# Performance work log

Hardware: AMD Instinct MI355X
Metric: run time of the kernel (lower is better)

Reference implementation:

```python
import jax, jax.numpy as jnp
from jax import lax
import numpy as np

NHEAD = 8
GROUPS = 32


def _conv2d(x, w, b=None, stride=1, pad=1):
    y = lax.conv_general_dilated(x, w, (stride, stride), ((pad, pad), (pad, pad)),
                                 dimension_numbers=('NCHW', 'OIHW', 'NCHW'))
    return y if b is None else y + b[None, :, None, None]


def _xcorr(x, k):
    # depthwise cross-correlation: batch*channel groups
    b, c, H, W = x.shape
    y = lax.conv_general_dilated(x.reshape(1, b * c, H, W),
                                 k.reshape(b * c, 1, k.shape[2], k.shape[3]),
                                 (1, 1), 'VALID', feature_group_count=b * c,
                                 dimension_numbers=('NCHW', 'OIHW', 'NCHW'))
    return y.reshape(b, c, y.shape[2], y.shape[3])


def _bn(x, g, b, m, v):
    inv = lax.rsqrt(v + 1e-5)
    return (x - m[None, :, None, None]) * (g * inv)[None, :, None, None] + b[None, :, None, None]


def _gn(x, g, b):
    B, C, H, W = x.shape
    xr = x.reshape(B, GROUPS, -1)
    mu = xr.mean(-1, keepdims=True)
    var = xr.var(-1, keepdims=True)
    xr = (xr - mu) * lax.rsqrt(var + 1e-5)
    return xr.reshape(B, C, H, W) * g[None, :, None, None] + b[None, :, None, None]


def _ln(x, g, b):
    mu = x.mean(-1, keepdims=True)
    var = x.var(-1, keepdims=True)
    return (x - mu) * lax.rsqrt(var + 1e-5) * g + b


def _mha(q, k, v, wq, bq, wk, bk, wv, bv, wo, bo, bias):
    N, B, C = q.shape
    D = C // NHEAD
    qh = (q @ wq.T + bq).reshape(N, B, NHEAD, D)
    kh = (k @ wk.T + bk).reshape(k.shape[0], B, NHEAD, D)
    vh = (v @ wv.T + bv).reshape(v.shape[0], B, NHEAD, D)
    att = jnp.einsum('nbhd,mbhd->bhnm', qh, kh) * (D ** -0.5)
    att = jax.nn.softmax(att + bias[None, None], axis=-1)  # local-window additive mask
    o = jnp.einsum('bhnm,mbhd->nbhd', att, vh).reshape(N, B, C)
    return o @ wo.T + bo


def _forward(mask_size, x0, x1, x2, z0, z1, z2,
             conv1_w, bn1_g, bn1_b, bn1_m, bn1_v,
             conv3_w, bn3_g, bn3_b, bn3_m, bn3_v,
             conv2_w, bn2_g, bn2_b, bn2_m, bn2_v,
             row_embed, col_embed,
             t_wq, t_bq, t_wk, t_bk, t_wv, t_bv, t_wo, t_bo,
             t_ln1_g, t_ln1_b, t_ff1_w, t_ff1_b, t_ff2_w, t_ff2_b, t_ln2_g, t_ln2_b,
             convloc_w, convloc_b, convloc_gn_g, convloc_gn_b, loc_out_w, loc_out_b,
             convcls_w, convcls_b, convcls_gn_g, convcls_gn_b,
             cls1_w, cls1_b, cls2_w, cls2_b):
    res1 = jax.nn.relu(_bn(_conv2d(_xcorr(x0, z0), conv1_w, None, 2, 1), bn1_g, bn1_b, bn1_m, bn1_v))
    res2 = jax.nn.relu(_bn(_conv2d(_xcorr(x1, z1), conv3_w, None, 2, 1), bn3_g, bn3_b, bn3_m, bn3_v))
    res3 = jax.nn.relu(_bn(_conv2d(_xcorr(x2, z2), conv2_w, None, 2, 1), bn2_g, bn2_b, bn2_m, bn2_v))

    b, c, W3, H3 = res3.shape
    # positional embedding: h,w = res3.shape[-2:]
    hh, ww = W3, H3
    x_emb = col_embed[:ww]            # (w, C/2)
    y_emb = row_embed[:hh]            # (h, C/2)
    half = c // 2
    pos_hw = jnp.concatenate([jnp.broadcast_to(x_emb[None], (hh, ww, half)),
                              jnp.broadcast_to(y_emb[:, None], (hh, ww, half))], -1)
    pos_seq = pos_hw.reshape(hh * ww, 1, c)  # (N,1,C), broadcasts over batch

    # local-window mask: position allowed iff both coord offsets <= mask_size//2
    ms2 = mask_size // 2
    idx = jnp.arange(W3 * H3)
    ri, ci = idx // H3, idx % H3
    allowed = (jnp.abs(ri[:, None] - ri[None, :]) <= ms2) & (jnp.abs(ci[:, None] - ci[None, :]) <= ms2)
    bias = jnp.where(allowed, 0.0, -1e9).astype(res3.dtype)

    src1 = res1.reshape(b, c, -1).transpose(2, 0, 1)  # (N,B,C)
    src2 = res2.reshape(b, c, -1).transpose(2, 0, 1)
    src3 = res3.reshape(b, c, -1).transpose(2, 0, 1)

    out = src3
    mems = (src1, src2)
    for li in range(2):  # 2 post-norm transformer layers (fixed structural loop)
        q = out + pos_seq
        kk = mems[li] + pos_seq
        a = _mha(q, kk, mems[li], t_wq[li], t_bq[li], t_wk[li], t_bk[li],
                 t_wv[li], t_bv[li], t_wo[li], t_bo[li], bias)
        out = _ln(out + a, t_ln1_g[li], t_ln1_b[li])
        ff = jax.nn.relu(out @ t_ff1_w[li].T + t_ff1_b[li]) @ t_ff2_w[li].T + t_ff2_b[li]
        out = _ln(out + ff, t_ln2_g[li], t_ln2_b[li])

    res = out.transpose(1, 2, 0).reshape(b, c, W3, H3)

    y = res
    for i in range(3):
        y = jax.nn.relu(_gn(_conv2d(y, convloc_w[i], convloc_b[i]), convloc_gn_g[i], convloc_gn_b[i]))
    loc = _conv2d(y, loc_out_w, loc_out_b)

    y = res
    for i in range(3):
        y = jax.nn.relu(_gn(_conv2d(y, convcls_w[i], convcls_b[i]), convcls_gn_g[i], convcls_gn_b[i]))
    cls1 = _conv2d(y, cls1_w, cls1_b)
    cls2 = _conv2d(y, cls2_w, cls2_b)
    return (loc, cls1, cls2)


def setup_inputs():
    key = jax.random.key(0)
    kit = iter(jax.random.split(key, 80))
    def nrm(shape, s=1.0):
        return (jax.random.normal(next(kit), shape) * s).astype(jnp.float32)
    def uni(shape):
        return jax.random.uniform(next(kit), shape, dtype=jnp.float32)
    d = {}
    d['x0'] = nrm((64, 384, 31, 31)); d['x1'] = nrm((64, 384, 31, 31)); d['x2'] = nrm((64, 256, 31, 31))
    d['z0'] = nrm((64, 384, 7, 7)); d['z1'] = nrm((64, 384, 7, 7)); d['z2'] = nrm((64, 256, 7, 7))
    d['conv1_w'] = nrm((192, 384, 3, 3), 0.01)
    d['conv3_w'] = nrm((192, 384, 3, 3), 0.02)
    d['conv2_w'] = nrm((192, 256, 3, 3), 0.02)
    for tag in ('1', '2', '3'):
        d['bn%s_g' % tag] = jnp.ones(192); d['bn%s_b' % tag] = jnp.zeros(192)
        d['bn%s_m' % tag] = jnp.zeros(192); d['bn%s_v' % tag] = jnp.ones(192)
    d['row_embed'] = uni((50, 96)); d['col_embed'] = uni((50, 96))
    for nm in ('q', 'k', 'v', 'o'):
        d['t_w%s' % nm] = nrm((2, 192, 192), 0.02); d['t_b%s' % nm] = jnp.zeros((2, 192))
    d['t_ln1_g'] = jnp.ones((2, 192)); d['t_ln1_b'] = jnp.zeros((2, 192))
    d['t_ln2_g'] = jnp.ones((2, 192)); d['t_ln2_b'] = jnp.zeros((2, 192))
    d['t_ff1_w'] = nrm((2, 768, 192), 0.02); d['t_ff1_b'] = jnp.zeros((2, 768))
    d['t_ff2_w'] = nrm((2, 192, 768), 0.02); d['t_ff2_b'] = jnp.zeros((2, 192))
    d['convloc_w'] = nrm((3, 192, 192, 3, 3), 0.02); d['convloc_b'] = jnp.zeros((3, 192))
    d['convloc_gn_g'] = jnp.ones((3, 192)); d['convloc_gn_b'] = jnp.zeros((3, 192))
    d['loc_out_w'] = nrm((4, 192, 3, 3), 0.02); d['loc_out_b'] = jnp.zeros(4)
    d['convcls_w'] = nrm((3, 192, 192, 3, 3), 0.02); d['convcls_b'] = jnp.zeros((3, 192))
    d['convcls_gn_g'] = jnp.ones((3, 192)); d['convcls_gn_b'] = jnp.zeros((3, 192))
    d['cls1_w'] = nrm((2, 192, 3, 3), 0.02); d['cls1_b'] = jnp.zeros(2)
    d['cls2_w'] = nrm((1, 192, 3, 3), 0.02); d['cls2_b'] = jnp.zeros(1)
    d['mask_size'] = 5
    return d


def reference(x0, x1, x2, z0, z1, z2,
              conv1_w, bn1_g, bn1_b, bn1_m, bn1_v,
              conv3_w, bn3_g, bn3_b, bn3_m, bn3_v,
              conv2_w, bn2_g, bn2_b, bn2_m, bn2_v,
              row_embed, col_embed,
              t_wq, t_bq, t_wk, t_bk, t_wv, t_bv, t_wo, t_bo,
              t_ln1_g, t_ln1_b, t_ff1_w, t_ff1_b, t_ff2_w, t_ff2_b, t_ln2_g, t_ln2_b,
              convloc_w, convloc_b, convloc_gn_g, convloc_gn_b, loc_out_w, loc_out_b,
              convcls_w, convcls_b, convcls_gn_g, convcls_gn_b,
              cls1_w, cls1_b, cls2_w, cls2_b, mask_size):
    return _forward(mask_size, x0, x1, x2, z0, z1, z2,
                    conv1_w, bn1_g, bn1_b, bn1_m, bn1_v,
                    conv3_w, bn3_g, bn3_b, bn3_m, bn3_v,
                    conv2_w, bn2_g, bn2_b, bn2_m, bn2_v,
                    row_embed, col_embed,
                    t_wq, t_bq, t_wk, t_bk, t_wv, t_bv, t_wo, t_bo,
                    t_ln1_g, t_ln1_b, t_ff1_w, t_ff1_b, t_ff2_w, t_ff2_b, t_ln2_g, t_ln2_b,
                    convloc_w, convloc_b, convloc_gn_g, convloc_gn_b, loc_out_w, loc_out_b,
                    convcls_w, convcls_b, convcls_gn_g, convcls_gn_b,
                    cls1_w, cls1_b, cls2_w, cls2_b)
```

## Files before the change

kernel.cpp:

```cpp
#include <hip/hip_runtime.h>
#include <cstdint>
#include <cstddef>

#define NB   64
#define C192 192
#define NPIX 169
#define WD   13
#define NH   8
#define HD   24
#define SEQM (NPIX*NB)

__global__ __launch_bounds__(256) void xcorr_kernel(
    const float* __restrict__ x, const float* __restrict__ z,
    float* __restrict__ out)
{
    int bc = blockIdx.x;
    const float* xin = x + (size_t)bc * 961;
    const float* zin = z + (size_t)bc * 49;
    float* o = out + (size_t)bc * 625;
    __shared__ float xs[961];
    __shared__ float zs[49];
    for (int i = threadIdx.x; i < 961; i += 256) xs[i] = xin[i];
    if (threadIdx.x < 49) zs[threadIdx.x] = zin[threadIdx.x];
    __syncthreads();
    for (int p = threadIdx.x; p < 625; p += 256) {
        int oy = p / 25, ox = p % 25;
        float acc = 0.f;
        #pragma unroll
        for (int ky = 0; ky < 7; ++ky) {
            #pragma unroll
            for (int kx = 0; kx < 7; ++kx)
                acc = fmaf(xs[(oy + ky) * 31 + ox + kx], zs[ky * 7 + kx], acc);
        }
        o[p] = acc;
    }
}

template<int CIN, int S, int HIN, bool TRANS_OUT>
__global__ __launch_bounds__(256) void conv_gemm(
    const float* __restrict__ in, const float* __restrict__ w,
    float* __restrict__ part)
{
    constexpr int KH = CIN / 2;
    constexpr int NT = KH / 4;
    __shared__ float smem[2 * 36 * 68];
    float* As = smem;
    float* Ws = smem + 36 * 68;
    const int m0 = blockIdx.x * 64;
    const int n0 = blockIdx.y * 64;
    const int kz = blockIdx.z;
    const int t  = threadIdx.x;
    const int lm = t & 63;
    const int lc = t >> 6;
    const int m  = m0 + lm;
    const int b  = m / NPIX;
    const int pix = m % NPIX;
    const int oy = pix / WD, ox = pix % WD;
    const int iy0 = S * oy - 1, ix0 = S * ox - 1;
    bool okY[3], okX[3];
    #pragma unroll
    for (int k = 0; k < 3; ++k) {
        okY[k] = (unsigned)(iy0 + k) < (unsigned)HIN;
        okX[k] = (unsigned)(ix0 + k) < (unsigned)HIN;
    }
    const float* pA = in + ((size_t)b * CIN + kz * KH + lc) * (HIN * HIN) + iy0 * HIN + ix0;
    const float* pW = w + ((size_t)(n0 + lm) * CIN + kz * KH + lc) * 9;
    const int tx = t & 15, ty = t >> 4;
    float acc[4][4] = {};
    float av[9], wv[9];
    #pragma unroll
    for (int ky = 0; ky < 3; ++ky)
        #pragma unroll
        for (int kx = 0; kx < 3; ++kx)
            av[ky * 3 + kx] = (okY[ky] && okX[kx]) ? pA[ky * HIN + kx] : 0.f;
    #pragma unroll
    for (int j = 0; j < 9; ++j) wv[j] = pW[j];

    for (int kt = 0; kt < NT; ++kt) {
        __syncthreads();
        {
            float* a  = As + (lc * 9) * 68 + lm;
            float* wd = Ws + (lc * 9) * 68 + lm;
            #pragma unroll
            for (int j = 0; j < 9; ++j) { a[j * 68] = av[j]; wd[j * 68] = wv[j]; }
        }
        __syncthreads();
        if (kt + 1 < NT) {
            pA += 4 * HIN * HIN;
            pW += 36;
            #pragma unroll
            for (int ky = 0; ky < 3; ++ky)
                #pragma unroll
                for (int kx = 0; kx < 3; ++kx)
                    av[ky * 3 + kx] = (okY[ky] && okX[kx]) ? pA[ky * HIN + kx] : 0.f;
            #pragma unroll
            for (int j = 0; j < 9; ++j) wv[j] = pW[j];
        }
        #pragma unroll
        for (int kk = 0; kk < 36; ++kk) {
            const float4 a4 = *(const float4*)&As[kk * 68 + ty * 4];
            const float4 w4 = *(const float4*)&Ws[kk * 68 + tx * 4];
            const float aa[4] = {a4.x, a4.y, a4.z, a4.w};
            const float wb[4] = {w4.x, w4.y, w4.z, w4.w};
            #pragma unroll
            for (int i = 0; i < 4; ++i)
                #pragma unroll
                for (int j = 0; j < 4; ++j)
                    acc[i][j] = fmaf(aa[i], wb[j], acc[i][j]);
        }
    }
    part += (size_t)kz * ((size_t)SEQM * C192);
    if (!TRANS_OUT) {
        #pragma unroll
        for (int i = 0; i < 4; ++i) {
            int mm = m0 + ty * 4 + i;
            float4 v = make_float4(acc[i][0], acc[i][1], acc[i][2], acc[i][3]);
            *(float4*)&part[(size_t)mm * C192 + n0 + tx * 4] = v;
        }
    } else {
        __syncthreads();
        float* Cl = smem;
        #pragma unroll
        for (int i = 0; i < 4; ++i)
            #pragma unroll
            for (int j = 0; j < 4; ++j)
                Cl[(tx * 4 + j) * 65 + ty * 4 + i] = acc[i][j];
        __syncthreads();
        #pragma unroll
        for (int rep = 0; rep < 16; ++rep) {
            int nl = rep * 4 + lc;
            part[((size_t)b * C192 + n0 + nl) * NPIX + pix] = Cl[nl * 65 + lm];
        }
    }
}

__global__ __launch_bounds__(256) void reduce_bn_relu(
    const float* __restrict__ p, const float* __restrict__ g,
    const float* __restrict__ bb, const float* __restrict__ mm,
    const float* __restrict__ vv, float* __restrict__ out)
{
    const int i = blockIdx.x * 256 + threadIdx.x;
    const int c4 = i % 48;
    const float4* p4 = (const float4*)p;
    float4 a = p4[i];
    float4 bpart = p4[i + (size_t)SEQM * 48];
    float4 g4 = *(const float4*)&g[c4 * 4];
    float4 b4 = *(const float4*)&bb[c4 * 4];
    float4 m4 = *(const float4*)&mm[c4 * 4];
    float4 v4 = *(const float4*)&vv[c4 * 4];
    float4 r;
    {
        float sc = g4.x * rsqrtf(v4.x + 1e-5f); r.x = fmaxf(fmaf(a.x + bpart.x - m4.x, sc, b4.x), 0.f);
    }
    { float sc = g4.y * rsqrtf(v4.y + 1e-5f); r.y = fmaxf(fmaf(a.y + bpart.y - m4.y, sc, b4.y), 0.f); }
    { float sc = g4.z * rsqrtf(v4.z + 1e-5f); r.z = fmaxf(fmaf(a.z + bpart.z - m4.z, sc, b4.z), 0.f); }
    { float sc = g4.w * rsqrtf(v4.w + 1e-5f); r.w = fmaxf(fmaf(a.w + bpart.w - m4.w, sc, b4.w), 0.f); }
    ((float4*)out)[i] = r;
}

__global__ __launch_bounds__(256) void gn_reduce_relu(
    const float* __restrict__ p, const float* __restrict__ cbias,
    const float* __restrict__ g, const float* __restrict__ bgn,
    float* __restrict__ out)
{
    const int blk = blockIdx.x;
    const int bb = blk / 32, grp = blk % 32;
    const size_t base = ((size_t)bb * C192 + grp * 6) * NPIX;
    const float* p0 = p + base;
    const float* p1 = p + (size_t)SEQM * C192 + base;
    const int N = 6 * NPIX;
    const int t = threadIdx.x;
    float vals[4];
    float s = 0.f, s2 = 0.f;
    #pragma unroll
    for (int i = 0; i < 4; ++i) {
        int idx = t + i * 256;
        float v = 0.f;
        if (idx < N) v = p0[idx] + p1[idx] + cbias[grp * 6 + idx / NPIX];
        vals[i] = v; s += v; s2 += v * v;
    }
    #pragma unroll
    for (int o = 32; o; o >>= 1) { s += __shfl_down(s, o); s2 += __shfl_down(s2, o); }
    __shared__ float redS[4], redS2[4];
    int wid = t >> 6, lane = t & 63;
    if (lane == 0) { redS[wid] = s; redS2[wid] = s2; }
    __syncthreads();
    float S  = redS[0] + redS[1] + redS[2] + redS[3];
    float S2 = redS2[0] + redS2[1] + redS2[2] + redS2[3];
    float mean = S / (float)N;
    float var  = S2 / (float)N - mean * mean;
    float inv  = rsqrtf(var + 1e-5f);
    #pragma unroll
    for (int i = 0; i < 4; ++i) {
        int idx = t + i * 256;
        if (idx < N) {
            int ch = grp * 6 + idx / NPIX;
            float y = (vals[i] - mean) * inv * g[ch] + bgn[ch];
            out[base + idx] = fmaxf(y, 0.f);
        }
    }
}

template<int CO_T>
__global__ __launch_bounds__(192) void conv_s1_bias(
    const float* __restrict__ in, const float* __restrict__ w,
    const float* __restrict__ bias, float* __restrict__ out)
{
    const int b    = blockIdx.x;
    const int co0  = blockIdx.y * CO_T;
    const int Cout = gridDim.y * CO_T;
    const int t    = threadIdx.x;
    __shared__ float xs[4 * 225];
    float acc[CO_T];
    #pragma unroll
    for (int i = 0; i < CO_T; ++i) acc[i] = 0.f;
    int py = 0, px = 0;
    if (t < NPIX) { py = t / WD; px = t % WD; }
    const float* inb = in + (size_t)b * C192 * NPIX;

    for (int c0 = 0; c0 < C192; c0 += 4) {
        __syncthreads();
        for (int i = t; i < 4 * 225; i += 192) {
            int pl = i / 225, pp = i % 225;
            int y = pp / 15, x = pp % 15;
            float v = 0.f;
            if (y >= 1 && y <= 13 && x >= 1 && x <= 13)
                v = inb[(size_t)(c0 + pl) * NPIX + (y - 1) * WD + (x - 1)];
            xs[i] = v;
        }
        __syncthreads();
        if (t < NPIX) {
            #pragma unroll
            for (int pl = 0; pl < 4; ++pl) {
                float xv[9];
                const float* xp = xs + pl * 225;
                #pragma unroll
                for (int ky = 0; ky < 3; ++ky) {
                    #pragma unroll
                    for (int kx = 0; kx < 3; ++kx)
                        xv[ky * 3 + kx] = xp[(py + ky) * 15 + px + kx];
                }
                #pragma unroll
                for (int co = 0; co < CO_T; ++co) {
                    const float* wc = w + ((size_t)(co0 + co) * C192 + (c0 + pl)) * 9;
                    #pragma unroll
                    for (int k = 0; k < 9; ++k)
                        acc[co] = fmaf(xv[k], wc[k], acc[co]);
                }
            }
        }
    }
    if (t < NPIX) {
        #pragma unroll
        for (int co = 0; co < CO_T; ++co) {
            int c = co0 + co;
            out[((size_t)b * Cout + c) * NPIX + t] = acc[co] + bias[c];
        }
    }
}

template<bool RELU>
__global__ __launch_bounds__(256) void gemm_nt(
    const float* __restrict__ A, const float* __restrict__ W,
    const float* __restrict__ bias, float* __restrict__ C,
    int M, int N, int K)
{
    const int BK = 32;
    __shared__ float As[BK][68];
    __shared__ float Ws[BK][68];
    const int mb = blockIdx.x, nb = blockIdx.y;
    const int t = threadIdx.x;
    const int tx = t % 16, ty = t / 16;
    float acc[4][4] = {};
    for (int k0 = 0; k0 < K; k0 += BK) {
        __syncthreads();
        {
            int r = t / 8, kv = (t % 8) * 4;
            const float4 a0 = *(const float4*)&A[(size_t)(mb * 64 + r) * K + k0 + kv];
            const float4 a1 = *(const float4*)&A[(size_t)(mb * 64 + r + 32) * K + k0 + kv];
            As[kv + 0][r] = a0.x; As[kv + 1][r] = a0.y; As[kv + 2][r] = a0.z; As[kv + 3][r] = a0.w;
            As[kv + 0][r + 32] = a1.x; As[kv + 1][r + 32] = a1.y; As[kv + 2][r + 32] = a1.z; As[kv + 3][r + 32] = a1.w;
            const float4 w0 = *(const float4*)&W[(size_t)(nb * 64 + r) * K + k0 + kv];
            const float4 w1 = *(const float4*)&W[(size_t)(nb * 64 + r + 32) * K + k0 + kv];
            Ws[kv + 0][r] = w0.x; Ws[kv + 1][r] = w0.y; Ws[kv + 2][r] = w0.z; Ws[kv + 3][r] = w0.w;
            Ws[kv + 0][r + 32] = w1.x; Ws[kv + 1][r + 32] = w1.y; Ws[kv + 2][r + 32] = w1.z; Ws[kv + 3][r + 32] = w1.w;
        }
        __syncthreads();
        #pragma unroll
        for (int kk = 0; kk < BK; ++kk) {
            const float4 a4 = *(const float4*)&As[kk][ty * 4];
            const float4 w4 = *(const float4*)&Ws[kk][tx * 4];
            const float aa[4] = {a4.x, a4.y, a4.z, a4.w};
            const float wb[4] = {w4.x, w4.y, w4.z, w4.w};
            #pragma unroll
            for (int i = 0; i < 4; ++i)
                #pragma unroll
                for (int j = 0; j < 4; ++j)
                    acc[i][j] = fmaf(aa[i], wb[j], acc[i][j]);
        }
    }
    const float4 bv = *(const float4*)&bias[nb * 64 + tx * 4];
    #pragma unroll
    for (int i = 0; i < 4; ++i) {
        int mrow = mb * 64 + ty * 4 + i;
        float4 v = make_float4(acc[i][0] + bv.x, acc[i][1] + bv.y,
                               acc[i][2] + bv.z, acc[i][3] + bv.w);
        if (RELU) { v.x = fmaxf(v.x, 0.f); v.y = fmaxf(v.y, 0.f); v.z = fmaxf(v.z, 0.f); v.w = fmaxf(v.w, 0.f); }
        *(float4*)&C[(size_t)mrow * N + nb * 64 + tx * 4] = v;
    }
}

__global__ __launch_bounds__(256) void addpos_kernel(
    const float* __restrict__ src, const float* __restrict__ row_e,
    const float* __restrict__ col_e, float* __restrict__ dst)
{
    const int total = SEQM * C192;
    int i = blockIdx.x * 256 + threadIdx.x;
    if (i >= total) return;
    int c = i % C192;
    int pix = (i / C192) % NPIX;
    float p = (c < 96) ? col_e[(pix % WD) * 96 + c] : row_e[(pix / WD) * 96 + (c - 96)];
    dst[i] = src[i] + p;
}

__global__ __launch_bounds__(192) void attn_kernel(
    const float* __restrict__ Q, const float* __restrict__ K,
    const float* __restrict__ V, const int* __restrict__ mask_size,
    float* __restrict__ O)
{
    const int bh = blockIdx.x;
    const int b = bh / NH, h = bh % NH;
    __shared__ float Ks[NPIX][HD];
    __shared__ float Vs[NPIX][HD];
    const int t = threadIdx.x;
    for (int i = t; i < NPIX * HD; i += 192) {
        int n = i / HD, d = i % HD;
        size_t base = ((size_t)b * NPIX + n) * C192 + h * HD + d;
        Ks[n][d] = K[base];
        Vs[n][d] = V[base];
    }
    __syncthreads();
    if (t < NPIX) {
        float q[HD];
        size_t qbase = ((size_t)b * NPIX + t) * C192 + h * HD;
        #pragma unroll
        for (int d = 0; d < HD; ++d) q[d] = Q[qbase + d];
        const int ms2 = mask_size[0] / 2;
        const int ri = t / WD, ci = t % WD;
        const int r0 = max(ri - ms2, 0), r1 = min(ri + ms2, WD - 1);
        const int c0 = max(ci - ms2, 0), c1 = min(ci + ms2, WD - 1);
        float mx = -1e30f, sum = 0.f;
        float o[HD];
        #pragma unroll
        for (int d = 0; d < HD; ++d) o[d] = 0.f;
        const float scale = 0.20412414523193150f;
        for (int rm = r0; rm <= r1; ++rm) {
            for (int cm = c0; cm <= c1; ++cm) {
                int m = rm * WD + cm;
                float s = 0.f;
                #pragma unroll
                for (int d = 0; d < HD; ++d) s = fmaf(q[d], Ks[m][d], s);
                s *= scale;
                if (s > mx) {
                    float f = expf(mx - s);
                    sum *= f;
                    #pragma unroll
                    for (int d = 0; d < HD; ++d) o[d] *= f;
                    mx = s;
                }
                float p = expf(s - mx);
                sum += p;
                #pragma unroll
                for (int d = 0; d < HD; ++d) o[d] = fmaf(p, Vs[m][d], o[d]);
            }
        }
        float r = 1.f / sum;
        #pragma unroll
        for (int d = 0; d < HD; ++d) O[qbase + d] = o[d] * r;
    }
}

__global__ __launch_bounds__(256) void add_ln_kernel(
    float* __restrict__ x, const float* __restrict__ a,
    const float* __restrict__ g, const float* __restrict__ b)
{
    const int row = blockIdx.x * 4 + (threadIdx.x >> 6);
    const int lane = threadIdx.x & 63;
    float* xp = x + (size_t)row * C192;
    const float* ap = a + (size_t)row * C192;
    float v[3];
    float s = 0.f, s2 = 0.f;
    #pragma unroll
    for (int i = 0; i < 3; ++i) {
        float t = xp[lane + i * 64] + ap[lane + i * 64];
        v[i] = t; s += t; s2 += t * t;
    }
    #pragma unroll
    for (int o = 32; o; o >>= 1) { s += __shfl_down(s, o); s2 += __shfl_down(s2, o); }
    s = __shfl(s, 0); s2 = __shfl(s2, 0);
    float mean = s * (1.f / 192.f);
    float var  = s2 * (1.f / 192.f) - mean * mean;
    float inv  = rsqrtf(var + 1e-5f);
    #pragma unroll
    for (int i = 0; i < 3; ++i) {
        int c = lane + i * 64;
        xp[c] = (v[i] - mean) * inv * g[c] + b[c];
    }
}

__global__ __launch_bounds__(256) void bpc_to_bcp(
    const float* __restrict__ src, float* __restrict__ dst)
{
    __shared__ float tile[32][33];
    const int b = blockIdx.z;
    const int n0 = blockIdx.x * 32, c0 = blockIdx.y * 32;
    const int tx = threadIdx.x % 32, ty = threadIdx.x / 32;
    #pragma unroll
    for (int i = 0; i < 32; i += 8) {
        int n = n0 + ty + i, c = c0 + tx;
        if (n < NPIX) tile[ty + i][tx] = src[((size_t)b * NPIX + n) * C192 + c];
    }
    __syncthreads();
    #pragma unroll
    for (int i = 0; i < 32; i += 8) {
        int c = c0 + ty + i, n = n0 + tx;
        if (n < NPIX) dst[((size_t)b * C192 + c) * NPIX + n] = tile[tx][ty + i];
    }
}

extern "C" void kernel_launch(void* const* d_in, const int* in_sizes, int n_in,
                              void* d_out, int out_size, void* d_ws, size_t ws_size,
                              hipStream_t stream)
{
    const float* x0 = (const float*)d_in[0];
    const float* x1 = (const float*)d_in[1];
    const float* x2 = (const float*)d_in[2];
    const float* z0 = (const float*)d_in[3];
    const float* z1 = (const float*)d_in[4];
    const float* z2 = (const float*)d_in[5];
    const float* conv1_w = (const float*)d_in[6];
    const float* conv3_w = (const float*)d_in[7];
    const float* conv2_w = (const float*)d_in[8];
    const float* bn1_g = (const float*)d_in[9];
    const float* bn1_b = (const float*)d_in[10];
    const float* bn1_m = (const float*)d_in[11];
    const float* bn1_v = (const float*)d_in[12];
    const float* bn2_g = (const float*)d_in[13];
    const float* bn2_b = (const float*)d_in[14];
    const float* bn2_m = (const float*)d_in[15];
    const float* bn2_v = (const float*)d_in[16];
    const float* bn3_g = (const float*)d_in[17];
    const float* bn3_b = (const float*)d_in[18];
    const float* bn3_m = (const float*)d_in[19];
    const float* bn3_v = (const float*)d_in[20];
    const float* row_embed = (const float*)d_in[21];
    const float* col_embed = (const float*)d_in[22];
    const float* t_wq = (const float*)d_in[23];
    const float* t_bq = (const float*)d_in[24];
    const float* t_wk = (const float*)d_in[25];
    const float* t_bk = (const float*)d_in[26];
    const float* t_wv = (const float*)d_in[27];
    const float* t_bv = (const float*)d_in[28];
    const float* t_wo = (const float*)d_in[29];
    const float* t_bo = (const float*)d_in[30];
    const float* t_ln1_g = (const float*)d_in[31];
    const float* t_ln1_b = (const float*)d_in[32];
    const float* t_ln2_g = (const float*)d_in[33];
    const float* t_ln2_b = (const float*)d_in[34];
    const float* t_ff1_w = (const float*)d_in[35];
    const float* t_ff1_b = (const float*)d_in[36];
    const float* t_ff2_w = (const float*)d_in[37];
    const float* t_ff2_b = (const float*)d_in[38];
    const float* convloc_w = (const float*)d_in[39];
    const float* convloc_b = (const float*)d_in[40];
    const float* convloc_gn_g = (const float*)d_in[41];
    const float* convloc_gn_b = (const float*)d_in[42];
    const float* loc_out_w = (const float*)d_in[43];
    const float* loc_out_b = (const float*)d_in[44];
    const float* convcls_w = (const float*)d_in[45];
    const float* convcls_b = (const float*)d_in[46];
    const float* convcls_gn_g = (const float*)d_in[47];
    const float* convcls_gn_b = (const float*)d_in[48];
    const float* cls1_w = (const float*)d_in[49];
    const float* cls1_b = (const float*)d_in[50];
    const float* cls2_w = (const float*)d_in[51];
    const float* cls2_b = (const float*)d_in[52];
    const int*   mask_size = (const int*)d_in[53];
    float* out = (float*)d_out;

    const size_t SZ_X = (size_t)NB * 384 * 625;
    const size_t SZ_S = (size_t)SEQM * C192;
    float* ws   = (float*)d_ws;
    float* Abuf = ws;
    float* res1 = Abuf + SZ_X;
    float* res2 = res1 + SZ_S;
    float* outb = res2 + SZ_S;
    float* qb   = outb + SZ_S;
    float* kb   = qb + SZ_S;
    float* vb   = kb + SZ_S;
    float* ob   = vb + SZ_S;
    float* resT = ob + SZ_S;
    float* y0   = resT + SZ_S;
    float* y1   = y0 + SZ_S;
    float* pbuf = qb;

    const dim3 cgrid(NPIX, 3, 2);
    const int  rgrid = SEQM * 48 / 256;
    const dim3 tgrid(6, 6, NB);

    xcorr_kernel<<<NB * 384, 256, 0, stream>>>(x0, z0, Abuf);
    conv_gemm<384, 2, 25, false><<<cgrid, 256, 0, stream>>>(Abuf, conv1_w, pbuf);
    reduce_bn_relu<<<rgrid, 256, 0, stream>>>(pbuf, bn1_g, bn1_b, bn1_m, bn1_v, res1);

    xcorr_kernel<<<NB * 384, 256, 0, stream>>>(x1, z1, Abuf);
    conv_gemm<384, 2, 25, false><<<cgrid, 256, 0, stream>>>(Abuf, conv3_w, pbuf);
    reduce_bn_relu<<<rgrid, 256, 0, stream>>>(pbuf, bn3_g, bn3_b, bn3_m, bn3_v, res2);

    xcorr_kernel<<<NB * 256, 256, 0, stream>>>(x2, z2, Abuf);
    conv_gemm<256, 2, 25, false><<<cgrid, 256, 0, stream>>>(Abuf, conv2_w, pbuf);
    reduce_bn_relu<<<rgrid, 256, 0, stream>>>(pbuf, bn2_g, bn2_b, bn2_m, bn2_v, outb);

    const int addpos_grid = (SEQM * C192 + 255) / 256;
    for (int li = 0; li < 2; ++li) {
        const float* mem = (li == 0) ? res1 : res2;
        const float* wq = t_wq + (size_t)li * C192 * C192;
        const float* wk = t_wk + (size_t)li * C192 * C192;
        const float* wv = t_wv + (size_t)li * C192 * C192;
        const float* wo = t_wo + (size_t)li * C192 * C192;
        const float* bq = t_bq + (size_t)li * C192;
        const float* bk = t_bk + (size_t)li * C192;
        const float* bv = t_bv + (size_t)li * C192;
        const float* bo = t_bo + (size_t)li * C192;

        addpos_kernel<<<addpos_grid, 256, 0, stream>>>(outb, row_embed, col_embed, qb);
        addpos_kernel<<<addpos_grid, 256, 0, stream>>>(mem,  row_embed, col_embed, kb);

        gemm_nt<false><<<dim3(SEQM / 64, 3), 256, 0, stream>>>(qb,  wq, bq, vb, SEQM, C192, C192);
        gemm_nt<false><<<dim3(SEQM / 64, 3), 256, 0, stream>>>(kb,  wk, bk, qb, SEQM, C192, C192);
        gemm_nt<false><<<dim3(SEQM / 64, 3), 256, 0, stream>>>(mem, wv, bv, kb, SEQM, C192, C192);

        attn_kernel<<<NB * NH, 192, 0, stream>>>(vb, qb, kb, mask_size, ob);

        gemm_nt<false><<<dim3(SEQM / 64, 3), 256, 0, stream>>>(ob, wo, bo, qb, SEQM, C192, C192);
        add_ln_kernel<<<SEQM / 4, 256, 0, stream>>>(outb, qb,
            t_ln1_g + (size_t)li * C192, t_ln1_b + (size_t)li * C192);

        gemm_nt<true><<<dim3(SEQM / 64, 12), 256, 0, stream>>>(outb,
            t_ff1_w + (size_t)li * 768 * C192, t_ff1_b + (size_t)li * 768, Abuf, SEQM, 768, C192);
        gemm_nt<false><<<dim3(SEQM / 64, 3), 256, 0, stream>>>(Abuf,
            t_ff2_w + (size_t)li * C192 * 768, t_ff2_b + (size_t)li * C192, qb, SEQM, C192, 768);
        add_ln_kernel<<<SEQM / 4, 256, 0, stream>>>(outb, qb,
            t_ln2_g + (size_t)li * C192, t_ln2_b + (size_t)li * C192);
    }

    bpc_to_bcp<<<tgrid, 256, 0, stream>>>(outb, resT);

    {
        const float* yin = resT;
        float* ybufs[2] = { y0, y1 };
        for (int i = 0; i < 3; ++i) {
            conv_gemm<192, 1, 13, true><<<cgrid, 256, 0, stream>>>(yin,
                convloc_w + (size_t)i * C192 * C192 * 9, pbuf);
            gn_reduce_relu<<<NB * 32, 256, 0, stream>>>(pbuf, convloc_b + (size_t)i * C192,
                convloc_gn_g + (size_t)i * C192, convloc_gn_b + (size_t)i * C192, ybufs[i & 1]);
            yin = ybufs[i & 1];
        }
        conv_s1_bias<4><<<dim3(NB, 1), 192, 0, stream>>>(yin, loc_out_w, loc_out_b, out);
    }

    {
        const float* yin = resT;
        float* ybufs[2] = { y1, y0 };
        for (int i = 0; i < 3; ++i) {
            conv_gemm<192, 1, 13, true><<<cgrid, 256, 0, stream>>>(yin,
                convcls_w + (size_t)i * C192 * C192 * 9, pbuf);
            gn_reduce_relu<<<NB * 32, 256, 0, stream>>>(pbuf, convcls_b + (size_t)i * C192,
                convcls_gn_g + (size_t)i * C192, convcls_gn_b + (size_t)i * C192, ybufs[i & 1]);
            yin = ybufs[i & 1];
        }
        conv_s1_bias<2><<<dim3(NB, 1), 192, 0, stream>>>(yin, cls1_w, cls1_b, out + (size_t)NB * 4 * NPIX);
        conv_s1_bias<1><<<dim3(NB, 1), 192, 0, stream>>>(yin, cls2_w, cls2_b, out + (size_t)NB * 6 * NPIX);
    }
}
```

Baseline: 2.509 ms.

## Move conv and transformer GEMMs to bf16x3 split MFMA

Replaces the FP32 FMA tiled conv-GEMM and linear-layer GEMM kernels with MFMA 16x16x32 bf16 kernels. Each operand is split into hi and lo bf16 parts and three products are summed to keep near-FP32 accuracy. Weights are pre-split into a chunked K-major bf16 layout by new kernels launched on every call, while activations are split on the fly into a swizzled LDS tile. The aim is to use the matrix cores for the dominant GEMM work. In exchange it adds the weight-split launches, workspace memory, a triple MFMA count and unvectorized scalar output stores.

```diff
diff --git a/kernel.cpp b/kernel.cpp
--- a/kernel.cpp
+++ b/kernel.cpp
@@ -9,6 +9,69 @@
 #define NH   8
 #define HD   24
 #define SEQM (NPIX*NB)
+
+typedef __attribute__((ext_vector_type(8))) short  s16x8;
+typedef __attribute__((ext_vector_type(4))) float  f32x4;
+
+__device__ __forceinline__ void split2(float x, unsigned short& h, unsigned short& l) {
+    unsigned int u = __float_as_uint(x);
+    unsigned int r = u + 0x7fffu + ((u >> 16) & 1u);
+    h = (unsigned short)(r >> 16);
+    float hf = __uint_as_float((unsigned int)h << 16);
+    float res = x - hf;
+    unsigned int u2 = __float_as_uint(res);
+    unsigned int r2 = u2 + 0x7fffu + ((u2 >> 16) & 1u);
+    l = (unsigned short)(r2 >> 16);
+}
+
+__global__ __launch_bounds__(256) void split_gemm_w(
+    const float* __restrict__ w, unsigned short* __restrict__ hi,
+    unsigned short* __restrict__ lo, int N, int K)
+{
+    int tid = blockIdx.x * 256 + threadIdx.x;
+    int K8 = K >> 3;
+    int n = tid / K8, kg8 = tid % K8;
+    int ck = kg8 >> 2, kgl = kg8 & 3;
+    const float* src = w + (size_t)n * K + kg8 * 8;
+    size_t dst = ((size_t)ck * N + n) * 32 + kgl * 8;
+    s16x8 h8, l8;
+    #pragma unroll
+    for (int j = 0; j < 8; ++j) {
+        unsigned short h, l; split2(src[j], h, l);
+        h8[j] = (short)h; l8[j] = (short)l;
+    }
+    *(s16x8*)(hi + dst) = h8;
+    *(s16x8*)(lo + dst) = l8;
+}
+
+template<int CIN, int CO>
+__global__ __launch_bounds__(256) void split_conv_w(
+    const float* __restrict__ w, unsigned short* __restrict__ hi,
+    unsigned short* __restrict__ lo)
+{
+    constexpr int CINh = CIN / 2;
+    constexpr int Klocal = 9 * CINh;
+    constexpr int K8 = Klocal / 8;
+    constexpr int NCH = Klocal / 32;
+    constexpr int CPK = CINh / 32;
+    int tid = blockIdx.x * 256 + threadIdx.x;
+    int kz = tid / (CO * K8);
+    int rem = tid % (CO * K8);
+    int n = rem / K8, kg8 = rem % K8;
+    int ck = kg8 >> 2, kgl = kg8 & 3;
+    int kidx = ck / CPK;
+    int cin0 = (ck % CPK) * 32 + kgl * 8;
+    s16x8 h8, l8;
+    #pragma unroll
+    for (int j = 0; j < 8; ++j) {
+        float v = w[((size_t)n * CIN + kz * CINh + cin0 + j) * 9 + kidx];
+        unsigned short h, l; split2(v, h, l);
+        h8[j] = (short)h; l8[j] = (short)l;
+    }
+    size_t dst = ((size_t)(kz * NCH + ck) * CO + n) * 32 + kgl * 8;
+    *(s16x8*)(hi + dst) = h8;
+    *(s16x8*)(lo + dst) = l8;
+}
 
 __global__ __launch_bounds__(256) void xcorr_kernel(
     const float* __restrict__ x, const float* __restrict__ z,
@@ -37,25 +100,29 @@
 }
 
 template<int CIN, int S, int HIN, bool TRANS_OUT>
-__global__ __launch_bounds__(256) void conv_gemm(
-    const float* __restrict__ in, const float* __restrict__ w,
+__global__ __launch_bounds__(256) void conv_mfma(
+    const float* __restrict__ in, const unsigned short* __restrict__ whi,
+    const unsigned short* __restrict__ wlo, int nstride, int noff,
     float* __restrict__ part)
 {
-    constexpr int KH = CIN / 2;
-    constexpr int NT = KH / 4;
-    __shared__ float smem[2 * 36 * 68];
-    float* As = smem;
-    float* Ws = smem + 36 * 68;
-    const int m0 = blockIdx.x * 64;
-    const int n0 = blockIdx.y * 64;
-    const int kz = blockIdx.z;
-    const int t  = threadIdx.x;
-    const int lm = t & 63;
-    const int lc = t >> 6;
-    const int m  = m0 + lm;
-    const int b  = m / NPIX;
-    const int pix = m % NPIX;
-    const int oy = pix / WD, ox = pix % WD;
+    constexpr int CINh = CIN / 2;
+    constexpr int NCH  = (9 * CINh) / 32;
+    constexpr int CPK  = CINh / 32;
+    constexpr int HIN2 = HIN * HIN;
+    __shared__ float smemf[4224];
+    unsigned short* Ahi = (unsigned short*)smemf;
+    unsigned short* Alo = Ahi + 2048;
+
+    const int t = threadIdx.x;
+    const int l = t & 63, wave = t >> 6;
+    const int mh = wave & 1, nh = wave >> 1;
+    const int lm16 = l & 15, kgl = l >> 4;
+    const int m0 = blockIdx.x * 64, n0 = blockIdx.y * 64, kz = blockIdx.z;
+
+    const int sm = t >> 2, skg = t & 3;
+    const int ms = m0 + sm;
+    const int bs = ms / NPIX, pixs = ms % NPIX;
+    const int oy = pixs / WD, ox = pixs % WD;
     const int iy0 = S * oy - 1, ix0 = S * ox - 1;
     bool okY[3], okX[3];
     #pragma unroll
@@ -63,74 +130,205 @@
         okY[k] = (unsigned)(iy0 + k) < (unsigned)HIN;
         okX[k] = (unsigned)(ix0 + k) < (unsigned)HIN;
     }
-    const float* pA = in + ((size_t)b * CIN + kz * KH + lc) * (HIN * HIN) + iy0 * HIN + ix0;
-    const float* pW = w + ((size_t)(n0 + lm) * CIN + kz * KH + lc) * 9;
-    const int tx = t & 15, ty = t >> 4;
-    float acc[4][4] = {};
-    float av[9], wv[9];
-    #pragma unroll
-    for (int ky = 0; ky < 3; ++ky)
-        #pragma unroll
-        for (int kx = 0; kx < 3; ++kx)
-            av[ky * 3 + kx] = (okY[ky] && okX[kx]) ? pA[ky * HIN + kx] : 0.f;
-    #pragma unroll
-    for (int j = 0; j < 9; ++j) wv[j] = pW[j];
-
-    for (int kt = 0; kt < NT; ++kt) {
+    const float* inb = in + ((size_t)bs * CIN + kz * CINh) * HIN2;
+    const int swz = sm * 32 + ((skg ^ ((sm >> 1) & 3)) * 8);
+
+    int ard[2];
+    #pragma unroll
+    for (int i = 0; i < 2; ++i) {
+        int m = mh * 32 + i * 16 + lm16;
+        ard[i] = m * 32 + ((kgl ^ ((m >> 1) & 3)) * 8);
+    }
+    size_t wof[2];
+    #pragma unroll
+    for (int jf = 0; jf < 2; ++jf) {
+        int n = noff + n0 + nh * 32 + jf * 16 + lm16;
+        wof[jf] = (size_t)n * 32 + kgl * 8;
+    }
+    const size_t kzbase = (size_t)kz * NCH;
+
+    f32x4 acc[2][2];
+    #pragma unroll
+    for (int i = 0; i < 2; ++i)
+        #pragma unroll
+        for (int j = 0; j < 2; ++j)
+            acc[i][j] = (f32x4){0.f, 0.f, 0.f, 0.f};
+
+    for (int ck = 0; ck < NCH; ++ck) {
+        const int kidx = ck / CPK;
+        const int cin0 = (ck % CPK) * 32;
+        const int ky = kidx / 3, kx = kidx % 3;
+        const unsigned short* wb  = whi + (kzbase + ck) * (size_t)nstride * 32;
+        const unsigned short* wbl = wlo + (kzbase + ck) * (size_t)nstride * 32;
+        s16x8 wh[2], wl[2];
+        #pragma unroll
+        for (int jf = 0; jf < 2; ++jf) {
+            wh[jf] = *(const s16x8*)(wb + wof[jf]);
+            wl[jf] = *(const s16x8*)(wbl + wof[jf]);
+        }
+        const bool ok = okY[ky] && okX[kx];
+        const float* src = inb + (size_t)(cin0 + skg * 8) * HIN2 + (iy0 + ky) * HIN + (ix0 + kx);
+        float av[8];
+        #pragma unroll
+        for (int j = 0; j < 8; ++j) av[j] = ok ? src[(size_t)j * HIN2] : 0.f;
+        s16x8 h8, l8;
+        #pragma unroll
+        for (int j = 0; j < 8; ++j) {
+            unsigned short h, lw; split2(av[j], h, lw);
+            h8[j] = (short)h; l8[j] = (short)lw;
+        }
         __syncthreads();
-        {
-            float* a  = As + (lc * 9) * 68 + lm;
-            float* wd = Ws + (lc * 9) * 68 + lm;
+        *(s16x8*)(Ahi + swz) = h8;
+        *(s16x8*)(Alo + swz) = l8;
+        __syncthreads();
+        s16x8 ah[2], al[2];
+        #pragma unroll
+        for (int i = 0; i < 2; ++i) {
+            ah[i] = *(const s16x8*)(Ahi + ard[i]);
+            al[i] = *(const s16x8*)(Alo + ard[i]);
+        }
+        #pragma unroll
+        for (int i = 0; i < 2; ++i)
             #pragma unroll
-            for (int j = 0; j < 9; ++j) { a[j * 68] = av[j]; wd[j * 68] = wv[j]; }
-        }
-        __syncthreads();
-        if (kt + 1 < NT) {
-            pA += 4 * HIN * HIN;
-            pW += 36;
-            #pragma unroll
-            for (int ky = 0; ky < 3; ++ky)
-                #pragma unroll
-                for (int kx = 0; kx < 3; ++kx)
-                    av[ky * 3 + kx] = (okY[ky] && okX[kx]) ? pA[ky * HIN + kx] : 0.f;
-            #pragma unroll
-            for (int j = 0; j < 9; ++j) wv[j] = pW[j];
-        }
-        #pragma unroll
-        for (int kk = 0; kk < 36; ++kk) {
-            const float4 a4 = *(const float4*)&As[kk * 68 + ty * 4];
-            const float4 w4 = *(const float4*)&Ws[kk * 68 + tx * 4];
-            const float aa[4] = {a4.x, a4.y, a4.z, a4.w};
-            const float wb[4] = {w4.x, w4.y, w4.z, w4.w};
-            #pragma unroll
-            for (int i = 0; i < 4; ++i)
-                #pragma unroll
-                for (int j = 0; j < 4; ++j)
-                    acc[i][j] = fmaf(aa[i], wb[j], acc[i][j]);
-        }
-    }
+            for (int jf = 0; jf < 2; ++jf) {
+                acc[i][jf] = __builtin_amdgcn_mfma_f32_16x16x32_bf16(ah[i], wl[jf], acc[i][jf], 0, 0, 0);
+                acc[i][jf] = __builtin_amdgcn_mfma_f32_16x16x32_bf16(al[i], wh[jf], acc[i][jf], 0, 0, 0);
+                acc[i][jf] = __builtin_amdgcn_mfma_f32_16x16x32_bf16(ah[i], wh[jf], acc[i][jf], 0, 0, 0);
+            }
+    }
+
     part += (size_t)kz * ((size_t)SEQM * C192);
     if (!TRANS_OUT) {
         #pragma unroll
-        for (int i = 0; i < 4; ++i) {
-            int mm = m0 + ty * 4 + i;
-            float4 v = make_float4(acc[i][0], acc[i][1], acc[i][2], acc[i][3]);
-            *(float4*)&part[(size_t)mm * C192 + n0 + tx * 4] = v;
-        }
+        for (int i = 0; i < 2; ++i)
+            #pragma unroll
+            for (int jf = 0; jf < 2; ++jf)
+                #pragma unroll
+                for (int r = 0; r < 4; ++r) {
+                    int m = m0 + mh * 32 + i * 16 + kgl * 4 + r;
+                    int n = n0 + nh * 32 + jf * 16 + lm16;
+                    part[(size_t)m * C192 + n] = acc[i][jf][r];
+                }
     } else {
         __syncthreads();
-        float* Cl = smem;
-        #pragma unroll
-        for (int i = 0; i < 4; ++i)
+        float* Cl = smemf;
+        #pragma unroll
+        for (int i = 0; i < 2; ++i)
             #pragma unroll
-            for (int j = 0; j < 4; ++j)
-                Cl[(tx * 4 + j) * 65 + ty * 4 + i] = acc[i][j];
+            for (int jf = 0; jf < 2; ++jf)
+                #pragma unroll
+                for (int r = 0; r < 4; ++r) {
+                    int ml = mh * 32 + i * 16 + kgl * 4 + r;
+                    int nl = nh * 32 + jf * 16 + lm16;
+                    Cl[nl * 65 + ml] = acc[i][jf][r];
+                }
         __syncthreads();
+        const int m_l = t & 63;
+        const int mm = m0 + m_l;
+        const int b2 = mm / NPIX, px2 = mm % NPIX;
         #pragma unroll
         for (int rep = 0; rep < 16; ++rep) {
-            int nl = rep * 4 + lc;
-            part[((size_t)b * C192 + n0 + nl) * NPIX + pix] = Cl[nl * 65 + lm];
-        }
+            int nl = rep * 4 + (t >> 6);
+            part[((size_t)b2 * C192 + n0 + nl) * NPIX + px2] = Cl[nl * 65 + m_l];
+        }
+    }
+}
+
+template<bool RELU>
+__global__ __launch_bounds__(256) void gemm_mfma(
+    const float* __restrict__ A, const unsigned short* __restrict__ whi,
+    const unsigned short* __restrict__ wlo, const float* __restrict__ bias,
+    float* __restrict__ C, int N, int K, int nstride, int noff)
+{
+    __shared__ unsigned short smem[4096];
+    unsigned short* Ahi = smem;
+    unsigned short* Alo = smem + 2048;
+    const int t = threadIdx.x;
+    const int l = t & 63, wave = t >> 6;
+    const int mh = wave & 1, nh = wave >> 1;
+    const int lm16 = l & 15, kgl = l >> 4;
+    const int m0 = blockIdx.x * 64, n0 = blockIdx.y * 64;
+    const int NCH = K >> 5;
+
+    const int sm = t >> 2, skg = t & 3;
+    const float* arow = A + (size_t)(m0 + sm) * K + skg * 8;
+    const int swz = sm * 32 + ((skg ^ ((sm >> 1) & 3)) * 8);
+
+    int ard[2];
+    #pragma unroll
+    for (int i = 0; i < 2; ++i) {
+        int m = mh * 32 + i * 16 + lm16;
+        ard[i] = m * 32 + ((kgl ^ ((m >> 1) & 3)) * 8);
+    }
+    size_t wof[2];
+    #pragma unroll
+    for (int jf = 0; jf < 2; ++jf) {
+        int n = noff + n0 + nh * 32 + jf * 16 + lm16;
+        wof[jf] = (size_t)n * 32 + kgl * 8;
+    }
+
+    f32x4 acc[2][2];
+    #pragma unroll
+    for (int i = 0; i < 2; ++i)
+        #pragma unroll
+        for (int j = 0; j < 2; ++j)
+            acc[i][j] = (f32x4){0.f, 0.f, 0.f, 0.f};
+
+    for (int ck = 0; ck < NCH; ++ck) {
+        const unsigned short* wb  = whi + (size_t)ck * nstride * 32;
+        const unsigned short* wbl = wlo + (size_t)ck * nstride * 32;
+        s16x8 wh[2], wl[2];
+        #pragma unroll
+        for (int jf = 0; jf < 2; ++jf) {
+            wh[jf] = *(const s16x8*)(wb + wof[jf]);
+            wl[jf] = *(const s16x8*)(wbl + wof[jf]);
+        }
+        float av[8];
+        {
+            const float4 a0 = *(const float4*)(arow + ck * 32);
+            const float4 a1 = *(const float4*)(arow + ck * 32 + 4);
+            av[0] = a0.x; av[1] = a0.y; av[2] = a0.z; av[3] = a0.w;
+            av[4] = a1.x; av[5] = a1.y; av[6] = a1.z; av[7] = a1.w;
+        }
+        s16x8 h8, l8;
+        #pragma unroll
+        for (int j = 0; j < 8; ++j) {
+            unsigned short h, lw; split2(av[j], h, lw);
+            h8[j] = (short)h; l8[j] = (short)lw;
+        }
+        __syncthreads();
+        *(s16x8*)(Ahi + swz) = h8;
+        *(s16x8*)(Alo + swz) = l8;
+        __syncthreads();
+        s16x8 ah[2], al[2];
+        #pragma unroll
+        for (int i = 0; i < 2; ++i) {
+            ah[i] = *(const s16x8*)(Ahi + ard[i]);
+            al[i] = *(const s16x8*)(Alo + ard[i]);
+        }
+        #pragma unroll
+        for (int i = 0; i < 2; ++i)
+            #pragma unroll
+            for (int jf = 0; jf < 2; ++jf) {
+                acc[i][jf] = __builtin_amdgcn_mfma_f32_16x16x32_bf16(ah[i], wl[jf], acc[i][jf], 0, 0, 0);
+                acc[i][jf] = __builtin_amdgcn_mfma_f32_16x16x32_bf16(al[i], wh[jf], acc[i][jf], 0, 0, 0);
+                acc[i][jf] = __builtin_amdgcn_mfma_f32_16x16x32_bf16(ah[i], wh[jf], acc[i][jf], 0, 0, 0);
+            }
+    }
+
+    #pragma unroll
+    for (int jf = 0; jf < 2; ++jf) {
+        int n = n0 + nh * 32 + jf * 16 + lm16;
+        float bv = bias[n];
+        #pragma unroll
+        for (int i = 0; i < 2; ++i)
+            #pragma unroll
+            for (int r = 0; r < 4; ++r) {
+                int m = m0 + mh * 32 + i * 16 + kgl * 4 + r;
+                float v = acc[i][jf][r] + bv;
+                if (RELU) v = fmaxf(v, 0.f);
+                C[(size_t)m * N + n] = v;
+            }
     }
 }
 
@@ -149,9 +347,7 @@
     float4 m4 = *(const float4*)&mm[c4 * 4];
     float4 v4 = *(const float4*)&vv[c4 * 4];
     float4 r;
-    {
-        float sc = g4.x * rsqrtf(v4.x + 1e-5f); r.x = fmaxf(fmaf(a.x + bpart.x - m4.x, sc, b4.x), 0.f);
-    }
+    { float sc = g4.x * rsqrtf(v4.x + 1e-5f); r.x = fmaxf(fmaf(a.x + bpart.x - m4.x, sc, b4.x), 0.f); }
     { float sc = g4.y * rsqrtf(v4.y + 1e-5f); r.y = fmaxf(fmaf(a.y + bpart.y - m4.y, sc, b4.y), 0.f); }
     { float sc = g4.z * rsqrtf(v4.z + 1e-5f); r.z = fmaxf(fmaf(a.z + bpart.z - m4.z, sc, b4.z), 0.f); }
     { float sc = g4.w * rsqrtf(v4.w + 1e-5f); r.w = fmaxf(fmaf(a.w + bpart.w - m4.w, sc, b4.w), 0.f); }
@@ -256,57 +452,6 @@
             int c = co0 + co;
             out[((size_t)b * Cout + c) * NPIX + t] = acc[co] + bias[c];
         }
-    }
-}
-
-template<bool RELU>
-__global__ __launch_bounds__(256) void gemm_nt(
-    const float* __restrict__ A, const float* __restrict__ W,
-    const float* __restrict__ bias, float* __restrict__ C,
-    int M, int N, int K)
-{
-    const int BK = 32;
-    __shared__ float As[BK][68];
-    __shared__ float Ws[BK][68];
-    const int mb = blockIdx.x, nb = blockIdx.y;
-    const int t = threadIdx.x;
-    const int tx = t % 16, ty = t / 16;
-    float acc[4][4] = {};
-    for (int k0 = 0; k0 < K; k0 += BK) {
-        __syncthreads();
-        {
-            int r = t / 8, kv = (t % 8) * 4;
-            const float4 a0 = *(const float4*)&A[(size_t)(mb * 64 + r) * K + k0 + kv];
-            const float4 a1 = *(const float4*)&A[(size_t)(mb * 64 + r + 32) * K + k0 + kv];
-            As[kv + 0][r] = a0.x; As[kv + 1][r] = a0.y; As[kv + 2][r] = a0.z; As[kv + 3][r] = a0.w;
-            As[kv + 0][r + 32] = a1.x; As[kv + 1][r + 32] = a1.y; As[kv + 2][r + 32] = a1.z; As[kv + 3][r + 32] = a1.w;
-            const float4 w0 = *(const float4*)&W[(size_t)(nb * 64 + r) * K + k0 + kv];
-            const float4 w1 = *(const float4*)&W[(size_t)(nb * 64 + r + 32) * K + k0 + kv];
-            Ws[kv + 0][r] = w0.x; Ws[kv + 1][r] = w0.y; Ws[kv + 2][r] = w0.z; Ws[kv + 3][r] = w0.w;
-            Ws[kv + 0][r + 32] = w1.x; Ws[kv + 1][r + 32] = w1.y; Ws[kv + 2][r + 32] = w1.z; Ws[kv + 3][r + 32] = w1.w;
-        }
-        __syncthreads();
-        #pragma unroll
-        for (int kk = 0; kk < BK; ++kk) {
-            const float4 a4 = *(const float4*)&As[kk][ty * 4];
-            const float4 w4 = *(const float4*)&Ws[kk][tx * 4];
-            const float aa[4] = {a4.x, a4.y, a4.z, a4.w};
-            const float wb[4] = {w4.x, w4.y, w4.z, w4.w};
-            #pragma unroll
-            for (int i = 0; i < 4; ++i)
-                #pragma unroll
-                for (int j = 0; j < 4; ++j)
-                    acc[i][j] = fmaf(aa[i], wb[j], acc[i][j]);
-        }
-    }
-    const float4 bv = *(const float4*)&bias[nb * 64 + tx * 4];
-    #pragma unroll
-    for (int i = 0; i < 4; ++i) {
-        int mrow = mb * 64 + ty * 4 + i;
-        float4 v = make_float4(acc[i][0] + bv.x, acc[i][1] + bv.y,
-                               acc[i][2] + bv.z, acc[i][3] + bv.w);
-        if (RELU) { v.x = fmaxf(v.x, 0.f); v.y = fmaxf(v.y, 0.f); v.z = fmaxf(v.z, 0.f); v.w = fmaxf(v.w, 0.f); }
-        *(float4*)&C[(size_t)mrow * N + nb * 64 + tx * 4] = v;
     }
 }
 
@@ -504,51 +649,74 @@
     float* y1   = y0 + SZ_S;
     float* pbuf = qb;
 
+    unsigned short* UB = (unsigned short*)(y1 + SZ_S);
+    size_t o = 0;
+    unsigned short* cw1h = UB + o; o += 663552; unsigned short* cw1l = UB + o; o += 663552;
+    unsigned short* cw3h = UB + o; o += 663552; unsigned short* cw3l = UB + o; o += 663552;
+    unsigned short* cw2h = UB + o; o += 442368; unsigned short* cw2l = UB + o; o += 442368;
+    unsigned short* cwlh = UB + o; o += 995328; unsigned short* cwll = UB + o; o += 995328;
+    unsigned short* cwch = UB + o; o += 995328; unsigned short* cwcl = UB + o; o += 995328;
+    unsigned short* twqh = UB + o; o += 73728;  unsigned short* twql = UB + o; o += 73728;
+    unsigned short* twkh = UB + o; o += 73728;  unsigned short* twkl = UB + o; o += 73728;
+    unsigned short* twvh = UB + o; o += 73728;  unsigned short* twvl = UB + o; o += 73728;
+    unsigned short* twoh = UB + o; o += 73728;  unsigned short* twol = UB + o; o += 73728;
+    unsigned short* tf1h = UB + o; o += 294912; unsigned short* tf1l = UB + o; o += 294912;
+    unsigned short* tf2h = UB + o; o += 294912; unsigned short* tf2l = UB + o; o += 294912;
+
+    split_conv_w<384, 192><<<324, 256, 0, stream>>>(conv1_w, cw1h, cw1l);
+    split_conv_w<384, 192><<<324, 256, 0, stream>>>(conv3_w, cw3h, cw3l);
+    split_conv_w<256, 192><<<216, 256, 0, stream>>>(conv2_w, cw2h, cw2l);
+    split_conv_w<192, 576><<<486, 256, 0, stream>>>(convloc_w, cwlh, cwll);
+    split_conv_w<192, 576><<<486, 256, 0, stream>>>(convcls_w, cwch, cwcl);
+    split_gemm_w<<<36, 256, 0, stream>>>(t_wq, twqh, twql, 384, 192);
+    split_gemm_w<<<36, 256, 0, stream>>>(t_wk, twkh, twkl, 384, 192);
+    split_gemm_w<<<36, 256, 0, stream>>>(t_wv, twvh, twvl, 384, 192);
+    split_gemm_w<<<36, 256, 0, stream>>>(t_wo, twoh, twol, 384, 192);
+    split_gemm_w<<<144, 256, 0, stream>>>(t_ff1_w, tf1h, tf1l, 1536, 192);
+    split_gemm_w<<<144, 256, 0, stream>>>(t_ff2_w, tf2h, tf2l, 384, 768);
+
     const dim3 cgrid(NPIX, 3, 2);
     const int  rgrid = SEQM * 48 / 256;
     const dim3 tgrid(6, 6, NB);
 
     xcorr_kernel<<<NB * 384, 256, 0, stream>>>(x0, z0, Abuf);
-    conv_gemm<384, 2, 25, false><<<cgrid, 256, 0, stream>>>(Abuf, conv1_w, pbuf);
+    conv_mfma<384, 2, 25, false><<<cgrid, 256, 0, stream>>>(Abuf, cw1h, cw1l, 192, 0, pbuf);
     reduce_bn_relu<<<rgrid, 256, 0, stream>>>(pbuf, bn1_g, bn1_b, bn1_m, bn1_v, res1);
 
     xcorr_kernel<<<NB * 384, 256, 0, stream>>>(x1, z1, Abuf);
-    conv_gemm<384, 2, 25, false><<<cgrid, 256, 0, stream>>>(Abuf, conv3_w, pbuf);
+    conv_mfma<384, 2, 25, false><<<cgrid, 256, 0, stream>>>(Abuf, cw3h, cw3l, 192, 0, pbuf);
     reduce_bn_relu<<<rgrid, 256, 0, stream>>>(pbuf, bn3_g, bn3_b, bn3_m, bn3_v, res2);
 
     xcorr_kernel<<<NB * 256, 256, 0, stream>>>(x2, z2, Abuf);
-    conv_gemm<256, 2, 25, false><<<cgrid, 256, 0, stream>>>(Abuf, conv2_w, pbuf);
+    conv_mfma<256, 2, 25, false><<<cgrid, 256, 0, stream>>>(Abuf, cw2h, cw2l, 192, 0, pbuf);
     reduce_bn_relu<<<rgrid, 256, 0, stream>>>(pbuf, bn2_g, bn2_b, bn2_m, bn2_v, outb);
 
     const int addpos_grid = (SEQM * C192 + 255) / 256;
     for (int li = 0; li < 2; ++li) {
         const float* mem = (li == 0) ? res1 : res2;
-        const float* wq = t_wq + (size_t)li * C192 * C192;
-        const float* wk = t_wk + (size_t)li * C192 * C192;
-        const float* wv = t_wv + (size_t)li * C192 * C192;
-        const float* wo = t_wo + (size_t)li * C192 * C192;
         const float* bq = t_bq + (size_t)li * C192;
         const float* bk = t_bk + (size_t)li * C192;
         const float* bv = t_bv + (size_t)li * C192;
         const float* bo = t_bo + (size_t)li * C192;
+        const int noff = li * C192;
 
         addpos_kernel<<<addpos_grid, 256, 0, stream>>>(outb, row_embed, col_embed, qb);
         addpos_kernel<<<addpos_grid, 256, 0, stream>>>(mem,  row_embed, col_embed, kb);
 
-        gemm_nt<false><<<dim3(SEQM / 64, 3), 256, 0, stream>>>(qb,  wq, bq, vb, SEQM, C192, C192);
-        gemm_nt<false><<<dim3(SEQM / 64, 3), 256, 0, stream>>>(kb,  wk, bk, qb, SEQM, C192, C192);
-        gemm_nt<false><<<dim3(SEQM / 64, 3), 256, 0, stream>>>(mem, wv, bv, kb, SEQM, C192, C192);
+        gemm_mfma<false><<<dim3(NPIX, 3), 256, 0, stream>>>(qb,  twqh, twql, bq, vb, 192, 192, 384, noff);
+        gemm_mfma<false><<<dim3(NPIX, 3), 256, 0, stream>>>(kb,  twkh, twkl, bk, qb, 192, 192, 384, noff);
+        gemm_mfma<false><<<dim3(NPIX, 3), 256, 0, stream>>>(mem, twvh, twvl, bv, kb, 192, 192, 384, noff);
 
         attn_kernel<<<NB * NH, 192, 0, stream>>>(vb, qb, kb, mask_size, ob);
 
-        gemm_nt<false><<<dim3(SEQM / 64, 3), 256, 0, stream>>>(ob, wo, bo, qb, SEQM, C192, C192);
+        gemm_mfma<false><<<dim3(NPIX, 3), 256, 0, stream>>>(ob, twoh, twol, bo, qb, 192, 192, 384, noff);
         add_ln_kernel<<<SEQM / 4, 256, 0, stream>>>(outb, qb,
             t_ln1_g + (size_t)li * C192, t_ln1_b + (size_t)li * C192);
 
-        gemm_nt<true><<<dim3(SEQM / 64, 12), 256, 0, stream>>>(outb,
-            t_ff1_w + (size_t)li * 768 * C192, t_ff1_b + (size_t)li * 768, Abuf, SEQM, 768, C192);
-        gemm_nt<false><<<dim3(SEQM / 64, 3), 256, 0, stream>>>(Abuf,
-            t_ff2_w + (size_t)li * C192 * 768, t_ff2_b + (size_t)li * C192, qb, SEQM, C192, 768);
+        gemm_mfma<true><<<dim3(NPIX, 12), 256, 0, stream>>>(outb, tf1h, tf1l,
+            t_ff1_b + (size_t)li * 768, Abuf, 768, 192, 1536, li * 768);
+        gemm_mfma<false><<<dim3(NPIX, 3), 256, 0, stream>>>(Abuf, tf2h, tf2l,
+            t_ff2_b + (size_t)li * C192, qb, 192, 768, 384, noff);
         add_ln_kernel<<<SEQM / 4, 256, 0, stream>>>(outb, qb,
             t_ln2_g + (size_t)li * C192, t_ln2_b + (size_t)li * C192);
     }
@@ -559,8 +727,7 @@
         const float* yin = resT;
         float* ybufs[2] = { y0, y1 };
         for (int i = 0; i < 3; ++i) {
-            conv_gemm<192, 1, 13, true><<<cgrid, 256, 0, stream>>>(yin,
-                convloc_w + (size_t)i * C192 * C192 * 9, pbuf);
+            conv_mfma<192, 1, 13, true><<<cgrid, 256, 0, stream>>>(yin, cwlh, cwll, 576, i * C192, pbuf);
             gn_reduce_relu<<<NB * 32, 256, 0, stream>>>(pbuf, convloc_b + (size_t)i * C192,
                 convloc_gn_g + (size_t)i * C192, convloc_gn_b + (size_t)i * C192, ybufs[i & 1]);
             yin = ybufs[i & 1];
@@ -572,8 +739,7 @@
         const float* yin = resT;
         float* ybufs[2] = { y1, y0 };
         for (int i = 0; i < 3; ++i) {
-            conv_gemm<192, 1, 13, true><<<cgrid, 256, 0, stream>>>(yin,
-                convcls_w + (size_t)i * C192 * C192 * 9, pbuf);
+            conv_mfma<192, 1, 13, true><<<cgrid, 256, 0, stream>>>(yin, cwch, cwcl, 576, i * C192, pbuf);
             gn_reduce_relu<<<NB * 32, 256, 0, stream>>>(pbuf, convcls_b + (size_t)i * C192,
                 convcls_gn_g + (size_t)i * C192, convcls_gn_b + (size_t)i * C192, ybufs[i & 1]);
             yin = ybufs[i & 1];
```

Result: faster. 2.282 ms (-9.0%).
